# Performance work log

Measured on AMD Instinct MI355X. Metric: run time of the kernel, lower is better.

The kernel has to match this reference:

```python
import jax, jax.numpy as jnp
import numpy as np

B, K, N, NBR = 4, 2048, 8192, 32
DIM, C_IN, W_HID, C_MID, F_HID, C_OUT = 3, 16, 32, 16, 64, 64
BIG = 3000.0


def _mlp(x, w1, b1, w2, b2):
    # SetTransform with one hidden layer, reduction='none': Linear->ReLU->Linear
    return jnp.maximum(x @ w1 + b1, 0.0) @ w2 + b2


def setup_inputs() -> dict:
    key = jax.random.key(0)
    ks = jax.random.split(key, 12)
    s = lambda fan_in: 1.0 / np.sqrt(fan_in)
    return {
        "keys": jax.random.normal(ks[0], (B, K, DIM), jnp.float32),
        "points": jax.random.normal(ks[1], (B, N, DIM), jnp.float32),
        "feats": jax.random.normal(ks[2], (B, N, C_IN), jnp.float32),
        "valid": jax.random.bernoulli(ks[3], 0.95, (B, K, N)),
        "ww1": jax.random.normal(ks[4], (DIM, W_HID), jnp.float32) * s(DIM),
        "wb1": jax.random.normal(ks[5], (W_HID,), jnp.float32) * s(DIM),
        "ww2": jax.random.normal(ks[6], (W_HID, C_MID), jnp.float32) * s(W_HID),
        "wb2": jax.random.normal(ks[7], (C_MID,), jnp.float32) * s(W_HID),
        "fw1": jax.random.normal(ks[8], (C_IN * C_MID, F_HID), jnp.float32) * s(C_IN * C_MID),
        "fb1": jax.random.normal(ks[9], (F_HID,), jnp.float32) * s(C_IN * C_MID),
        "fw2": jax.random.normal(ks[10], (F_HID, C_OUT), jnp.float32) * s(F_HID),
        "fb2": jax.random.normal(ks[11], (C_OUT,), jnp.float32) * s(F_HID),
    }


def reference(keys, points, feats, valid, ww1, wb1, ww2, wb2, fw1, fb1, fw2, fb2):
    # --- dist_fn (Euclidean): dist_vec = points - keys, dist = ||dist_vec|| ---
    diff = points[:, None, :, :] - keys[:, :, None, :]        # [B,K,N,DIM]
    dist = jnp.sqrt(jnp.sum(diff * diff, axis=-1))            # [B,K,N]
    big_dist = dist.max() * BIG
    dist = dist + jnp.where(valid, 0.0, big_dist)
    # --- kNN: smallest NBR distances per key ---
    _, idxs = jax.lax.top_k(-dist, NBR)                       # [B,K,NBR]
    bidx = jnp.arange(B)[:, None, None]
    # gather neighbor info (avoids materializing [B,K,N,*] gathered copies)
    n_rel = points[bidx, idxs] - keys[:, :, None, :]          # [B,K,NBR,DIM]
    n_feats = feats[bidx, idxs]                               # [B,K,NBR,C_IN]
    n_valid = jnp.take_along_axis(valid, idxs, axis=2)        # [B,K,NBR]
    n_valid = n_valid[..., None].astype(n_rel.dtype)
    # per-neighbor weight MLP, mask, batched matmul reduce over neighbors
    m = _mlp(n_rel, ww1, wb1, ww2, wb2) * n_valid             # [B,K,NBR,C_MID]
    nf = n_feats * n_valid                                    # [B,K,NBR,C_IN]
    e = jnp.einsum('bkqm,bkqc->bkmc', m, nf)                  # [B,K,C_MID,C_IN]
    e = e.reshape(B, K, C_MID * C_IN)
    return _mlp(e, fw1, fb1, fw2, fb2)                        # [B,K,C_OUT]
```

## Files before the change

### kernel.cpp

```cpp
#include <hip/hip_runtime.h>
#include <hip/hip_bf16.h>
#include <cstdint>
#include <cstddef>

#define B_    4
#define K_    2048
#define N_    8192
#define NBR_  32
#define NCAND 44
#define CIN   16
#define WHID  32
#define CMID  16
#define FHID  64
#define COUT  64

__global__ void pc_detect_kernel(const unsigned* __restrict__ v, int* __restrict__ flag) {
    const unsigned w = v[threadIdx.x & 63];
    const int byte_like = (((w & 0xFEFEFEFEu) == 0u) && ((w & 0xFFFFFF00u) != 0u)) ? 1 : 0;
    const unsigned long long m = __ballot(byte_like);
    if (threadIdx.x == 0) *flag = (m != 0ull) ? 1 : 0;
}

__device__ __forceinline__ unsigned umin_(unsigned a, unsigned b) { return a < b ? a : b; }
__device__ __forceinline__ unsigned umax_(unsigned a, unsigned b) { return a < b ? b : a; }

__device__ __forceinline__ void insert8(unsigned (&sa)[8], unsigned kv) {
    if (kv < sa[7]) {
#pragma unroll
        for (int i = 0; i < 8; ++i) {
            unsigned lo = umin_(sa[i], kv);
            kv = umax_(sa[i], kv);
            sa[i] = lo;
        }
    }
}

__device__ __forceinline__ void scan_pts4(const float* __restrict__ pts,
                                          float kx, float ky, float kz,
                                          int lane, unsigned (&sa)[8]) {
    const int l4 = lane * 4;
#pragma unroll 2
    for (int t = 0; t < N_ / 256; ++t) {
        const int n0 = t * 256 + l4;
        const float4* p4 = (const float4*)(pts + (size_t)n0 * 3);
        const float4 A  = p4[0];
        const float4 Bv = p4[1];
        const float4 Cv = p4[2];
        float dx, dy, dz, d2;
        dx = A.x - kx; dy = A.y - ky; dz = A.z - kz;
        d2 = fmaf(dz, dz, fmaf(dy, dy, dx * dx));
        const unsigned kv0 = (__float_as_uint(d2) & 0xFFFFE000u) | (unsigned)(n0 + 0);
        dx = A.w - kx; dy = Bv.x - ky; dz = Bv.y - kz;
        d2 = fmaf(dz, dz, fmaf(dy, dy, dx * dx));
        const unsigned kv1 = (__float_as_uint(d2) & 0xFFFFE000u) | (unsigned)(n0 + 1);
        dx = Bv.z - kx; dy = Bv.w - ky; dz = Cv.x - kz;
        d2 = fmaf(dz, dz, fmaf(dy, dy, dx * dx));
        const unsigned kv2 = (__float_as_uint(d2) & 0xFFFFE000u) | (unsigned)(n0 + 2);
        dx = Cv.y - kx; dy = Cv.z - ky; dz = Cv.w - kz;
        d2 = fmaf(dz, dz, fmaf(dy, dy, dx * dx));
        const unsigned kv3 = (__float_as_uint(d2) & 0xFFFFE000u) | (unsigned)(n0 + 3);
        insert8(sa, kv0);
        insert8(sa, kv1);
        insert8(sa, kv2);
        insert8(sa, kv3);
    }
}

struct Slice {
    union {
        unsigned cand[8 * 64];
        float    w[NBR_ * CMID];
        float    pad_[512];
    } A;
    union {
        float nf[NBR_ * CIN];
        struct { float hp[4 * FHID]; float hf[FHID]; } h;
    } Bv;
    union {
        unsigned slot[NBR_];
        float    e[CMID * CIN];
    } C;
};

__global__ __launch_bounds__(128, 8) void pc_main_kernel(
    const float* __restrict__ keys,
    const float* __restrict__ points,
    const float* __restrict__ feats,
    const void*  __restrict__ validp,
    const float* __restrict__ ww1, const float* __restrict__ wb1,
    const float* __restrict__ ww2, const float* __restrict__ wb2,
    const float* __restrict__ fw1, const float* __restrict__ fb1,
    const float* __restrict__ fw2, const float* __restrict__ fb2,
    float* __restrict__ out,
    const int* __restrict__ flagp)
{
    __shared__ Slice sl[2];

    const int lane = threadIdx.x & 63;
    const int wv   = threadIdx.x >> 6;
    const int row  = (blockIdx.x << 1) | wv;
    const int b    = row >> 11;
    Slice& S = sl[wv];

    const float kx = keys[row * 3 + 0];
    const float ky = keys[row * 3 + 1];
    const float kz = keys[row * 3 + 2];
    const float* pts = points + (size_t)b * N_ * 3;

    unsigned sa[8];
#pragma unroll
    for (int i = 0; i < 8; ++i) sa[i] = 0xFFFFFFFFu;

    scan_pts4(pts, kx, ky, kz, lane, sa);

#pragma unroll
    for (int i = 0; i < 8; ++i) S.A.cand[i * 64 + lane] = sa[i];
    __syncthreads();

    unsigned cur   = sa[0];
    int      head  = 0;
    unsigned mykey = 0xFFFFFFFFu;
#pragma unroll 4
    for (int r = 0; r < NCAND; ++r) {
        unsigned t = cur;
#pragma unroll
        for (int off = 1; off < 64; off <<= 1)
            t = umin_(t, (unsigned)__shfl_xor((int)t, off, 64));
        if (lane == r) mykey = t;
        if (cur == t) {
            ++head;
            cur = (head < 8) ? S.A.cand[head * 64 + lane] : 0xFFFFFFFFu;
        }
    }

    if (lane < NBR_) S.C.slot[lane] = 0xFFFFFFFFu;
    __syncthreads();

    {
        const int  cidx = (int)(mykey & 8191u);
        const float cdx = pts[cidx * 3 + 0] - kx;
        const float cdy = pts[cidx * 3 + 1] - ky;
        const float cdz = pts[cidx * 3 + 2] - kz;
        const float cd2 = fmaf(cdz, cdz, fmaf(cdy, cdy, cdx * cdx));
        const int flag = *flagp;
        const size_t vbase = (size_t)row * N_;
        unsigned vbit;
        if (flag) vbit = ((const unsigned char*)validp)[vbase + (size_t)cidx];
        else      vbit = ((const unsigned*)validp)[vbase + (size_t)cidx];
        const unsigned d2bits = (vbit != 0u) ? __float_as_uint(cd2) : 0xFFFFFFFFu;
        const unsigned long long fkey =
            ((unsigned long long)d2bits << 13) | (unsigned long long)cidx;
        int rank = 0;
#pragma unroll 11
        for (int j = 0; j < NCAND; ++j) {
            const unsigned long long fj = (unsigned long long)__shfl((long long)fkey, j, 64);
            rank += (fj < fkey) ? 1 : 0;
        }
        if (lane < NCAND && (vbit != 0u) && rank < NBR_)
            S.C.slot[rank] = mykey;
    }
    __syncthreads();

    const int q    = lane & 31;
    const int half = lane >> 5;
    const unsigned skey = S.C.slot[q];
    const int   nidx = (int)(skey & 8191u);
    const float vf   = (skey < 0xF0000000u) ? 1.0f : 0.0f;

    const float rx = pts[nidx * 3 + 0] - kx;
    const float ry = pts[nidx * 3 + 1] - ky;
    const float rz = pts[nidx * 3 + 2] - kz;

    float wacc[8];
    {
        const float4 b0 = *(const float4*)&wb2[half * 8 + 0];
        const float4 b1 = *(const float4*)&wb2[half * 8 + 4];
        wacc[0] = b0.x; wacc[1] = b0.y; wacc[2] = b0.z; wacc[3] = b0.w;
        wacc[4] = b1.x; wacc[5] = b1.y; wacc[6] = b1.z; wacc[7] = b1.w;
    }

#pragma unroll 8
    for (int j = 0; j < WHID; ++j) {
        float hj = fmaf(rx, ww1[j], fmaf(ry, ww1[WHID + j], fmaf(rz, ww1[2 * WHID + j], wb1[j])));
        hj = fmaxf(hj, 0.0f);
        const float4 wa = *(const float4*)&ww2[j * CMID + half * 8 + 0];
        const float4 wb = *(const float4*)&ww2[j * CMID + half * 8 + 4];
        wacc[0] = fmaf(hj, wa.x, wacc[0]);
        wacc[1] = fmaf(hj, wa.y, wacc[1]);
        wacc[2] = fmaf(hj, wa.z, wacc[2]);
        wacc[3] = fmaf(hj, wa.w, wacc[3]);
        wacc[4] = fmaf(hj, wb.x, wacc[4]);
        wacc[5] = fmaf(hj, wb.y, wacc[5]);
        wacc[6] = fmaf(hj, wb.z, wacc[6]);
        wacc[7] = fmaf(hj, wb.w, wacc[7]);
    }
#pragma unroll
    for (int m = 0; m < 8; ++m) wacc[m] *= vf;

    *(float4*)&S.A.w[q * CMID + half * 8 + 0] = make_float4(wacc[0], wacc[1], wacc[2], wacc[3]);
    *(float4*)&S.A.w[q * CMID + half * 8 + 4] = make_float4(wacc[4], wacc[5], wacc[6], wacc[7]);

    const float* fp = feats + ((size_t)b * N_ + (size_t)nidx) * CIN + half * 8;
    *(float4*)&S.Bv.nf[q * CIN + half * 8 + 0] = *(const float4*)(fp + 0);
    *(float4*)&S.Bv.nf[q * CIN + half * 8 + 4] = *(const float4*)(fp + 4);
    __syncthreads();

    {
        const int m  = lane >> 2;
        const int c4 = lane & 3;
        float4 eacc = make_float4(0.f, 0.f, 0.f, 0.f);
#pragma unroll
        for (int qq = 0; qq < NBR_; ++qq) {
            const float  wq = S.A.w[qq * CMID + m];
            const float4 f  = *(const float4*)&S.Bv.nf[qq * CIN + c4 * 4];
            eacc.x = fmaf(wq, f.x, eacc.x);
            eacc.y = fmaf(wq, f.y, eacc.y);
            eacc.z = fmaf(wq, f.z, eacc.z);
            eacc.w = fmaf(wq, f.w, eacc.w);
        }
        *(float4*)&S.C.e[m * CIN + c4 * 4] = eacc;
    }
    __syncthreads();

    {
        const int g  = lane >> 4;
        const int t4 = lane & 15;
        float a0 = 0.f, a1 = 0.f, a2 = 0.f, a3 = 0.f;
#pragma unroll 8
        for (int i = 0; i < 64; ++i) {
            const float  ev = S.C.e[g * 64 + i];
            const float4 wv2 = *(const float4*)&fw1[(size_t)(g * 64 + i) * FHID + t4 * 4];
            a0 = fmaf(ev, wv2.x, a0);
            a1 = fmaf(ev, wv2.y, a1);
            a2 = fmaf(ev, wv2.z, a2);
            a3 = fmaf(ev, wv2.w, a3);
        }
        *(float4*)&S.Bv.h.hp[g * FHID + t4 * 4] = make_float4(a0, a1, a2, a3);
    }
    __syncthreads();

    {
        float hf = fb1[lane] + S.Bv.h.hp[lane] + S.Bv.h.hp[FHID + lane]
                 + S.Bv.h.hp[2 * FHID + lane] + S.Bv.h.hp[3 * FHID + lane];
        S.Bv.h.hf[lane] = fmaxf(hf, 0.0f);
    }
    __syncthreads();

    {
        float oacc = fb2[lane];
#pragma unroll 8
        for (int j = 0; j < FHID; ++j)
            oacc = fmaf(S.Bv.h.hf[j], fw2[(size_t)j * COUT + lane], oacc);
        out[(size_t)row * COUT + lane] = oacc;
    }
}

extern "C" void kernel_launch(void* const* d_in, const int* in_sizes, int n_in,
                              void* d_out, int out_size, void* d_ws, size_t ws_size,
                              hipStream_t stream) {
    const float* keys   = (const float*)d_in[0];
    const float* points = (const float*)d_in[1];
    const float* feats  = (const float*)d_in[2];
    const void*  valid  = d_in[3];
    const float* ww1 = (const float*)d_in[4];
    const float* wb1 = (const float*)d_in[5];
    const float* ww2 = (const float*)d_in[6];
    const float* wb2 = (const float*)d_in[7];
    const float* fw1 = (const float*)d_in[8];
    const float* fb1 = (const float*)d_in[9];
    const float* fw2 = (const float*)d_in[10];
    const float* fb2 = (const float*)d_in[11];
    float* out = (float*)d_out;
    int*   flag = (int*)d_ws;

    pc_detect_kernel<<<1, 64, 0, stream>>>((const unsigned*)valid, flag);
    pc_main_kernel<<<(B_ * K_) / 2, 128, 0, stream>>>(keys, points, feats, valid,
                                                      ww1, wb1, ww2, wb2,
                                                      fw1, fb1, fw2, fb2,
                                                      out, flag);
}
```

Measured before the change: 413.3 us.

## Transpose points to SoA in workspace and use branchless med3 top-8 insertion

Adds a pre-pass kernel that transposes the point cloud into a structure-of-arrays layout in the workspace, so the kNN scan can load 8 points per lane with contiguous float4 reads. It also replaces the conditional sorted-insert with a branchless insertion built on v_med3_u32, one med3 per slot. This removes divergence and the compare/swap pairs in the hot scan loop, at the cost of an extra kernel launch and a round trip of the points through global memory. If the workspace is too small, the code falls back to the original AoS scan.

```diff
diff --git a/kernel.cpp b/kernel.cpp
--- a/kernel.cpp
+++ b/kernel.cpp
@@ -13,6 +13,8 @@
 #define CMID  16
 #define FHID  64
 #define COUT  64
+#define SOA_OFF 4096
+#define WS_NEED ((size_t)SOA_OFF + (size_t)B_ * 3 * N_ * 4)
 
 __global__ void pc_detect_kernel(const unsigned* __restrict__ v, int* __restrict__ flag) {
     const unsigned w = v[threadIdx.x & 63];
@@ -21,21 +23,63 @@
     if (threadIdx.x == 0) *flag = (m != 0ull) ? 1 : 0;
 }
 
+__global__ __launch_bounds__(256) void pc_soa_kernel(const float* __restrict__ pts,
+                                                     float* __restrict__ soa) {
+    const int i = blockIdx.x * 256 + threadIdx.x;
+    const int b = i >> 13, n = i & (N_ - 1);
+    const float* p = pts + (size_t)i * 3;
+    const float x = p[0], y = p[1], z = p[2];
+    float* d = soa + (size_t)b * 3 * N_ + n;
+    d[0]      = x;
+    d[N_]     = y;
+    d[2 * N_] = z;
+}
+
 __device__ __forceinline__ unsigned umin_(unsigned a, unsigned b) { return a < b ? a : b; }
 __device__ __forceinline__ unsigned umax_(unsigned a, unsigned b) { return a < b ? b : a; }
 
-__device__ __forceinline__ void insert8(unsigned (&sa)[8], unsigned kv) {
-    if (kv < sa[7]) {
-#pragma unroll
-        for (int i = 0; i < 8; ++i) {
-            unsigned lo = umin_(sa[i], kv);
-            kv = umax_(sa[i], kv);
-            sa[i] = lo;
-        }
-    }
-}
-
-__device__ __forceinline__ void scan_pts4(const float* __restrict__ pts,
+__device__ __forceinline__ unsigned med3_(unsigned a, unsigned b, unsigned c) {
+    unsigned d;
+    asm("v_med3_u32 %0, %1, %2, %3" : "=v"(d) : "v"(a), "v"(b), "v"(c));
+    return d;
+}
+__device__ __forceinline__ void insert_m3(unsigned (&sa)[8], unsigned kv) {
+#pragma unroll
+    for (int i = 7; i >= 1; --i)
+        sa[i] = med3_(sa[i - 1], sa[i], kv);
+    sa[0] = umin_(sa[0], kv);
+}
+
+__device__ __forceinline__ void scan_soa8(const float* __restrict__ px,
+                                          const float* __restrict__ py,
+                                          const float* __restrict__ pz,
+                                          float kx, float ky, float kz,
+                                          int lane, unsigned (&sa)[8]) {
+    const int l8 = lane * 8;
+#pragma unroll 2
+    for (int t = 0; t < N_ / 512; ++t) {
+        const int n0 = t * 512 + l8;
+        const float4 x0 = *(const float4*)(px + n0), x1 = *(const float4*)(px + n0 + 4);
+        const float4 y0 = *(const float4*)(py + n0), y1 = *(const float4*)(py + n0 + 4);
+        const float4 z0 = *(const float4*)(pz + n0), z1 = *(const float4*)(pz + n0 + 4);
+        float dx, dy, dz, d2;
+#define PC_ONE(J, XX, YY, ZZ)                                                        \
+        dx = XX - kx; dy = YY - ky; dz = ZZ - kz;                                    \
+        d2 = fmaf(dz, dz, fmaf(dy, dy, dx * dx));                                    \
+        insert_m3(sa, (__float_as_uint(d2) & 0xFFFFE000u) | (unsigned)(n0 + J));
+        PC_ONE(0, x0.x, y0.x, z0.x)
+        PC_ONE(1, x0.y, y0.y, z0.y)
+        PC_ONE(2, x0.z, y0.z, z0.z)
+        PC_ONE(3, x0.w, y0.w, z0.w)
+        PC_ONE(4, x1.x, y1.x, z1.x)
+        PC_ONE(5, x1.y, y1.y, z1.y)
+        PC_ONE(6, x1.z, y1.z, z1.z)
+        PC_ONE(7, x1.w, y1.w, z1.w)
+#undef PC_ONE
+    }
+}
+
+__device__ __forceinline__ void scan_aos4(const float* __restrict__ pts,
                                           float kx, float ky, float kz,
                                           int lane, unsigned (&sa)[8]) {
     const int l4 = lane * 4;
@@ -43,26 +87,20 @@
     for (int t = 0; t < N_ / 256; ++t) {
         const int n0 = t * 256 + l4;
         const float4* p4 = (const float4*)(pts + (size_t)n0 * 3);
-        const float4 A  = p4[0];
-        const float4 Bv = p4[1];
-        const float4 Cv = p4[2];
+        const float4 A = p4[0], Bv = p4[1], Cv = p4[2];
         float dx, dy, dz, d2;
         dx = A.x - kx; dy = A.y - ky; dz = A.z - kz;
         d2 = fmaf(dz, dz, fmaf(dy, dy, dx * dx));
-        const unsigned kv0 = (__float_as_uint(d2) & 0xFFFFE000u) | (unsigned)(n0 + 0);
+        insert_m3(sa, (__float_as_uint(d2) & 0xFFFFE000u) | (unsigned)(n0 + 0));
         dx = A.w - kx; dy = Bv.x - ky; dz = Bv.y - kz;
         d2 = fmaf(dz, dz, fmaf(dy, dy, dx * dx));
-        const unsigned kv1 = (__float_as_uint(d2) & 0xFFFFE000u) | (unsigned)(n0 + 1);
+        insert_m3(sa, (__float_as_uint(d2) & 0xFFFFE000u) | (unsigned)(n0 + 1));
         dx = Bv.z - kx; dy = Bv.w - ky; dz = Cv.x - kz;
         d2 = fmaf(dz, dz, fmaf(dy, dy, dx * dx));
-        const unsigned kv2 = (__float_as_uint(d2) & 0xFFFFE000u) | (unsigned)(n0 + 2);
+        insert_m3(sa, (__float_as_uint(d2) & 0xFFFFE000u) | (unsigned)(n0 + 2));
         dx = Cv.y - kx; dy = Cv.z - ky; dz = Cv.w - kz;
         d2 = fmaf(dz, dz, fmaf(dy, dy, dx * dx));
-        const unsigned kv3 = (__float_as_uint(d2) & 0xFFFFE000u) | (unsigned)(n0 + 3);
-        insert8(sa, kv0);
-        insert8(sa, kv1);
-        insert8(sa, kv2);
-        insert8(sa, kv3);
+        insert_m3(sa, (__float_as_uint(d2) & 0xFFFFE000u) | (unsigned)(n0 + 3));
     }
 }
 
@@ -82,9 +120,11 @@
     } C;
 };
 
+template <int SOA>
 __global__ __launch_bounds__(128, 8) void pc_main_kernel(
     const float* __restrict__ keys,
     const float* __restrict__ points,
+    const float* __restrict__ soa,
     const float* __restrict__ feats,
     const void*  __restrict__ validp,
     const float* __restrict__ ww1, const float* __restrict__ wb1,
@@ -111,7 +151,12 @@
 #pragma unroll
     for (int i = 0; i < 8; ++i) sa[i] = 0xFFFFFFFFu;
 
-    scan_pts4(pts, kx, ky, kz, lane, sa);
+    if (SOA) {
+        const float* px = soa + (size_t)b * 3 * N_;
+        scan_soa8(px, px + N_, px + 2 * N_, kx, ky, kz, lane, sa);
+    } else {
+        scan_aos4(pts, kx, ky, kz, lane, sa);
+    }
 
 #pragma unroll
     for (int i = 0; i < 8; ++i) S.A.cand[i * 64 + lane] = sa[i];
@@ -272,10 +317,18 @@
     const float* fb2 = (const float*)d_in[11];
     float* out = (float*)d_out;
     int*   flag = (int*)d_ws;
+    float* soa  = (float*)((char*)d_ws + SOA_OFF);
 
     pc_detect_kernel<<<1, 64, 0, stream>>>((const unsigned*)valid, flag);
-    pc_main_kernel<<<(B_ * K_) / 2, 128, 0, stream>>>(keys, points, feats, valid,
-                                                      ww1, wb1, ww2, wb2,
-                                                      fw1, fb1, fw2, fb2,
-                                                      out, flag);
-}
+
+    if (ws_size >= WS_NEED) {
+        pc_soa_kernel<<<(B_ * N_) / 256, 256, 0, stream>>>(points, soa);
+        pc_main_kernel<1><<<(B_ * K_) / 2, 128, 0, stream>>>(
+            keys, points, soa, feats, valid,
+            ww1, wb1, ww2, wb2, fw1, fb1, fw2, fb2, out, flag);
+    } else {
+        pc_main_kernel<0><<<(B_ * K_) / 2, 128, 0, stream>>>(
+            keys, points, soa, feats, valid,
+            ww1, wb1, ww2, wb2, fw1, fb1, fw2, fb2, out, flag);
+    }
+}
```

Result: faster. 396.4 us (-4.1%).
